# Performance work log

Measured on AMD Instinct MI355X. Metric: run time of the kernel, lower is better.

## Reference

```python
import jax, jax.numpy as jnp
import numpy as np

B, S, D, E, H, TOPK = 4, 2048, 1024, 32, 128, 4

def setup_inputs() -> dict:
    key = jax.random.key(0)
    k1, k2, k3, k4 = jax.random.split(key, 4)
    x = jax.random.normal(k1, (B, S, D), jnp.float32)
    expert_sel = jax.random.normal(k2, (E, D), jnp.float32) * (D ** -0.5)
    keys = jax.random.normal(k3, (E, D, H), jnp.float32) * (D ** -0.5)
    values = jax.random.normal(k4, (E, H, D), jnp.float32) * (H ** -0.5)
    return {"x": x, "expert_sel": expert_sel, "keys": keys, "values": values, "n_heads": TOPK}

def reference(x, expert_sel, keys, values, n_heads):
    # x: [B,S,D]; expert_sel: [E,D]; keys: [E,D,H]; values: [E,H,D]
    Bv, Sv, Dv = x.shape
    Ev = keys.shape[0]
    xf = x.reshape(-1, Dv)                                  # [N,D]
    N = xf.shape[0]
    gate = jax.nn.sigmoid(xf @ expert_sel.T)                # [N,E] sigmoid gating (sigma-MoE)
    vals, idx = jax.lax.top_k(gate, n_heads)                # [N,k] selected experts + gate weights
    # dense per-token-per-expert gate weights; zero for non-selected experts
    g = jnp.zeros((N, Ev), x.dtype).at[jnp.arange(N)[:, None], idx].set(vals)  # [N,E]
    # grouped expert FFN, expressed densely over the (small) expert axis:
    # out = sum_e g[n,e] * relu(x @ keys[e]) @ values[e]
    h = jax.nn.relu(jnp.einsum('nd,edh->enh', xf, keys))    # [E,N,H]
    out = jnp.einsum('enh,ehd->nd', h * g.T[:, :, None], values)  # [N,D]
    return out.reshape(Bv, Sv, Dv)
```

## Files before the change

kernel.cpp:

```cpp
#include <hip/hip_runtime.h>
#include <hip/hip_bf16.h>

#define NTOK 8192
#define DDIM 1024
#define NEXP 32
#define HDIM 128
#define TOPK 4

typedef __attribute__((ext_vector_type(8))) short bf16x8;
typedef __attribute__((ext_vector_type(4))) float f32x4;

typedef unsigned int uint_g __attribute__((address_space(1)));
typedef unsigned int uint_l __attribute__((address_space(3)));

__device__ __forceinline__ void async_cp16(const void* g, void* l) {
    __builtin_amdgcn_global_load_lds((const uint_g*)g, (uint_l*)l, 16, 0, 0);
}

__device__ inline unsigned short f2bf(float f) {
    unsigned int u = __builtin_bit_cast(unsigned int, f);
    unsigned int r = (u + 0x7fffu + ((u >> 16) & 1u)) >> 16;
    return (unsigned short)r;
}
__device__ inline float bf2f(unsigned short s) {
    unsigned int u = ((unsigned int)s) << 16;
    return __builtin_bit_cast(float, u);
}

__global__ __launch_bounds__(256) void prep_weights(
    const float* __restrict__ keys, const float* __restrict__ values,
    unsigned short* __restrict__ Kb, unsigned short* __restrict__ Vb)
{
    int idx = blockIdx.x * 256 + threadIdx.x;
    unsigned short o[8];
    if (idx < NEXP * 128 * 128) {
        int n = idx & 127, k0 = (idx >> 7) & 127, e = idx >> 14;
        const float* s = keys + ((size_t)e * DDIM + k0 * 8) * HDIM + n;
        #pragma unroll
        for (int j = 0; j < 8; ++j) o[j] = f2bf(s[(size_t)j * HDIM]);
        *(uint4*)&Kb[(size_t)idx * 8] = *(uint4*)o;
    } else {
        idx -= NEXP * 128 * 128;
        int n = idx & 1023, k0 = (idx >> 10) & 15, e = idx >> 14;
        const float* s = values + ((size_t)e * HDIM + k0 * 8) * DDIM + n;
        #pragma unroll
        for (int j = 0; j < 8; ++j) o[j] = f2bf(s[(size_t)j * DDIM]);
        *(uint4*)&Vb[(size_t)idx * 8] = *(uint4*)o;
    }
}

__global__ __launch_bounds__(256) void gate_partial(
    const float* __restrict__ x, const float* __restrict__ es,
    float* __restrict__ gpart)
{
    const int n0    = blockIdx.x * 16;
    const int dbase = blockIdx.y * 256;
    const int tid   = threadIdx.x;

    __shared__ float smem[4608];
    float* Xt  = smem;
    float* Est = smem + 64 * 36;

    const int t4  = (tid & 3) * 4;
    const int e4  = ((tid >> 2) & 7) * 4;
    const int rep = tid >> 5;

    const int xr = tid & 15, xc4 = (tid >> 4) * 4;
    const int er = tid & 31, ec8 = (tid >> 5) * 8;

    float acc[4][4] = {};

    for (int dc = dbase; dc < dbase + 256; dc += 64) {
        __syncthreads();
        {
            float4 v = *(const float4*)&x[(size_t)(n0 + xr) * DDIM + dc + xc4];
            Xt[(xc4 + 0) * 36 + xr] = v.x; Xt[(xc4 + 1) * 36 + xr] = v.y;
            Xt[(xc4 + 2) * 36 + xr] = v.z; Xt[(xc4 + 3) * 36 + xr] = v.w;
        }
        #pragma unroll
        for (int i = 0; i < 2; ++i) {
            float4 v = *(const float4*)&es[(size_t)er * DDIM + dc + ec8 + i * 4];
            Est[(ec8 + i * 4 + 0) * 36 + er] = v.x;
            Est[(ec8 + i * 4 + 1) * 36 + er] = v.y;
            Est[(ec8 + i * 4 + 2) * 36 + er] = v.z;
            Est[(ec8 + i * 4 + 3) * 36 + er] = v.w;
        }
        __syncthreads();

        #pragma unroll
        for (int s = 0; s < 8; ++s) {
            int d = s * 8 + rep;
            float4 xv = *(const float4*)&Xt[d * 36 + t4];
            float4 ev = *(const float4*)&Est[d * 36 + e4];
            const float xa[4] = {xv.x, xv.y, xv.z, xv.w};
            const float ea[4] = {ev.x, ev.y, ev.z, ev.w};
            #pragma unroll
            for (int i = 0; i < 4; ++i)
                #pragma unroll
                for (int j = 0; j < 4; ++j)
                    acc[i][j] = fmaf(xa[i], ea[j], acc[i][j]);
        }
    }

    __syncthreads();
    float* Lp = smem;
    #pragma unroll
    for (int i = 0; i < 4; ++i)
        #pragma unroll
        for (int j = 0; j < 4; ++j)
            Lp[(rep * 16 + t4 + i) * 33 + e4 + j] = acc[i][j];
    __syncthreads();

    for (int p = tid; p < 16 * 32; p += 256) {
        int tok = p >> 5, e = p & 31;
        float s = 0.f;
        #pragma unroll
        for (int r = 0; r < 8; ++r) s += Lp[(r * 16 + tok) * 33 + e];
        gpart[((size_t)blockIdx.y * NTOK + n0 + tok) * NEXP + e] = s;
    }
}

__global__ __launch_bounds__(256) void topk_scatter(
    const float* __restrict__ gpart,
    int* __restrict__ cnt, int* __restrict__ tok_list, float* __restrict__ gates)
{
    const int tid = threadIdx.x;
    const int n   = blockIdx.x * 256 + tid;

    __shared__ int hist[NEXP];
    __shared__ int bbase[NEXP];
    if (tid < NEXP) hist[tid] = 0;

    float lg[NEXP];
    #pragma unroll
    for (int i = 0; i < 8; ++i) {
        float4 v = *(const float4*)&gpart[(size_t)n * NEXP + i * 4];
        lg[i*4+0] = v.x; lg[i*4+1] = v.y; lg[i*4+2] = v.z; lg[i*4+3] = v.w;
    }
    #pragma unroll
    for (int j = 1; j < 4; ++j)
        #pragma unroll
        for (int i = 0; i < 8; ++i) {
            float4 v = *(const float4*)&gpart[((size_t)j * NTOK + n) * NEXP + i * 4];
            lg[i*4+0] += v.x; lg[i*4+1] += v.y; lg[i*4+2] += v.z; lg[i*4+3] += v.w;
        }

    int sel[TOPK]; float sv[TOPK];
    #pragma unroll
    for (int j = 0; j < TOPK; ++j) {
        float bv = -3.0e38f; int bi = 0;
        #pragma unroll
        for (int e = 0; e < NEXP; ++e) {
            bool taken = false;
            #pragma unroll
            for (int q = 0; q < j; ++q) taken = taken || (sel[q] == e);
            float v = taken ? -3.0e38f : lg[e];
            if (v > bv) { bv = v; bi = e; }
        }
        sel[j] = bi; sv[j] = bv;
    }

    __syncthreads();
    int lpos[TOPK];
    #pragma unroll
    for (int j = 0; j < TOPK; ++j) {
        gates[n * TOPK + j] = 1.f / (1.f + expf(-sv[j]));
        lpos[j] = atomicAdd(&hist[sel[j]], 1);
    }
    __syncthreads();
    if (tid < NEXP) bbase[tid] = atomicAdd(&cnt[tid], hist[tid]);
    __syncthreads();
    #pragma unroll
    for (int j = 0; j < TOPK; ++j)
        tok_list[(size_t)sel[j] * NTOK + bbase[sel[j]] + lpos[j]] = n * TOPK + j;
}

__global__ __launch_bounds__(256) void ffn_phase1(
    const float* __restrict__ x,
    const unsigned short* __restrict__ Kb,
    const int* __restrict__ cnt, const int* __restrict__ tok_list,
    const float* __restrict__ gates,
    unsigned short* __restrict__ Hb)
{
    const int e = blockIdx.y, tile = blockIdx.x;
    const int c = cnt[e], base = tile * 32;
    if (base >= c) return;
    const int nt   = min(32, c - base);
    const int tid  = threadIdx.x, wave = tid >> 6, lane = tid & 63;
    const int lm   = lane & 15, quad = lane >> 4;
    const int r2   = (wave >> 1) * 16, c2 = (wave & 1) * 64;

    __shared__ __align__(16) unsigned short Xs[32 * 72];
    __shared__ __align__(16) unsigned short Ks[8192];
    __shared__ int slot[32];
    __shared__ int toks[32];
    __shared__ float gs[32];

    if (tid < 32) {
        if (tid < nt) {
            int v = tok_list[(size_t)e * NTOK + base + tid];
            slot[tid] = v; toks[tid] = v >> 2; gs[tid] = gates[v];
        } else { slot[tid] = -1; toks[tid] = -1; gs[tid] = 0.f; }
    }
    __syncthreads();

    const unsigned short* Ke = Kb + (size_t)e * 131072;
    const int xr = tid >> 3, xseg = (tid & 7) * 8;
    const int xtok = toks[xr];
    const float* xrow = x + (size_t)(xtok < 0 ? 0 : xtok) * DDIM;

    f32x4 acc[4];
    #pragma unroll
    for (int j = 0; j < 4; ++j) acc[j] = (f32x4){0.f, 0.f, 0.f, 0.f};

    for (int dc = 0; dc < DDIM; dc += 64) {
        __syncthreads();
        #pragma unroll
        for (int i = 0; i < 4; ++i) {
            int u = wave * 4 + i;
            async_cp16(Ke + (size_t)dc * 128 + u * 512 + lane * 8, Ks + u * 512);
        }
        {
            float4 v0 = make_float4(0.f,0.f,0.f,0.f), v1 = v0;
            if (xtok >= 0) {
                v0 = *(const float4*)&xrow[dc + xseg];
                v1 = *(const float4*)&xrow[dc + xseg + 4];
            }
            unsigned short p[8] = { f2bf(v0.x), f2bf(v0.y), f2bf(v0.z), f2bf(v0.w),
                                    f2bf(v1.x), f2bf(v1.y), f2bf(v1.z), f2bf(v1.w) };
            *(uint4*)&Xs[xr * 72 + xseg] = *(uint4*)p;
        }
        __syncthreads();

        #pragma unroll
        for (int ks = 0; ks < 2; ++ks) {
            bf16x8 a = *(const bf16x8*)&Xs[(r2 + lm) * 72 + ks * 32 + quad * 8];
            #pragma unroll
            for (int tj = 0; tj < 4; ++tj) {
                bf16x8 b = *(const bf16x8*)&Ks[((ks * 4 + quad) * 128 + c2 + tj * 16 + lm) * 8];
                acc[tj] = __builtin_amdgcn_mfma_f32_16x16x32_bf16(a, b, acc[tj], 0, 0, 0);
            }
        }
    }

    #pragma unroll
    for (int reg = 0; reg < 4; ++reg) {
        int m = r2 + quad * 4 + reg;
        int s = slot[m];
        if (s >= 0) {
            float g = gs[m];
            unsigned short* hp = Hb + (size_t)s * HDIM;
            #pragma unroll
            for (int tj = 0; tj < 4; ++tj)
                hp[c2 + tj * 16 + lm] = f2bf(fmaxf(acc[tj][reg], 0.f) * g);
        }
    }
}

__global__ __launch_bounds__(256) void ffn_phase2(
    const unsigned short* __restrict__ Hb,
    const unsigned short* __restrict__ Vb,
    const int* __restrict__ cnt, const int* __restrict__ tok_list,
    unsigned short* __restrict__ Ob)
{
    const int e = blockIdx.z, nc = blockIdx.y, tile = blockIdx.x;
    const int c = cnt[e], base = tile * 64;
    if (base >= c) return;
    const int nt   = min(64, c - base);
    const int tid  = threadIdx.x, wave = tid >> 6, lane = tid & 63;
    const int lm   = lane & 15, quad = lane >> 4;
    const int r2   = (wave >> 1) * 32, c2 = (wave & 1) * 64;

    __shared__ __align__(16) unsigned short Hs[64 * 136];
    __shared__ __align__(16) unsigned short Vs[16384];
    __shared__ int slot[64];

    if (tid < 64) {
        if (tid < nt) slot[tid] = tok_list[(size_t)e * NTOK + base + tid];
        else          slot[tid] = -1;
    }
    __syncthreads();

    const unsigned short* Ve = Vb + (size_t)e * 131072;
    #pragma unroll
    for (int i = 0; i < 8; ++i) {
        int u = wave * 8 + i;
        int k0 = u >> 1, half = u & 1;
        async_cp16(Ve + ((size_t)k0 * 1024 + nc * 128 + half * 64 + lane) * 8,
                   Vs + u * 512);
    }
    {
        const int hr = tid >> 2, part = tid & 3;
        int s = slot[hr];
        uint4 z = {0u, 0u, 0u, 0u};
        uint4 d0 = z, d1 = z, d2 = z, d3 = z;
        if (s >= 0) {
            const uint4* src = (const uint4*)(Hb + (size_t)s * HDIM + part * 32);
            d0 = src[0]; d1 = src[1]; d2 = src[2]; d3 = src[3];
        }
        uint4* dst = (uint4*)&Hs[hr * 136 + part * 32];
        dst[0] = d0; dst[1] = d1; dst[2] = d2; dst[3] = d3;
    }
    __syncthreads();

    f32x4 acc[2][4];
    #pragma unroll
    for (int i = 0; i < 2; ++i)
        #pragma unroll
        for (int j = 0; j < 4; ++j) acc[i][j] = (f32x4){0.f, 0.f, 0.f, 0.f};

    #pragma unroll
    for (int ks = 0; ks < 4; ++ks) {
        bf16x8 a0 = *(const bf16x8*)&Hs[(r2 + lm) * 136 + ks * 32 + quad * 8];
        bf16x8 a1 = *(const bf16x8*)&Hs[(r2 + 16 + lm) * 136 + ks * 32 + quad * 8];
        #pragma unroll
        for (int tj = 0; tj < 4; ++tj) {
            bf16x8 b = *(const bf16x8*)&Vs[((ks * 4 + quad) * 128 + c2 + tj * 16 + lm) * 8];
            acc[0][tj] = __builtin_amdgcn_mfma_f32_16x16x32_bf16(a0, b, acc[0][tj], 0, 0, 0);
            acc[1][tj] = __builtin_amdgcn_mfma_f32_16x16x32_bf16(a1, b, acc[1][tj], 0, 0, 0);
        }
    }

    #pragma unroll
    for (int ti = 0; ti < 2; ++ti)
        #pragma unroll
        for (int reg = 0; reg < 4; ++reg) {
            int m = r2 + ti * 16 + quad * 4 + reg;
            int s = slot[m];
            if (s >= 0) {
                unsigned short* op = Ob + (size_t)s * DDIM + nc * 128 + c2 + lm;
                #pragma unroll
                for (int tj = 0; tj < 4; ++tj)
                    op[tj * 16] = f2bf(acc[ti][tj][reg]);
            }
        }
}

__global__ __launch_bounds__(256) void reduce_out(
    const unsigned short* __restrict__ Ob, float* __restrict__ out)
{
    const int tid = threadIdx.x;
    const int n   = blockIdx.x * 2 + (tid >> 7);
    const int cc  = (tid & 127) * 8;

    float s[8] = {};
    #pragma unroll
    for (int j = 0; j < 4; ++j) {
        uint4 v = *(const uint4*)&Ob[((size_t)n * 4 + j) * DDIM + cc];
        const unsigned int w[4] = {v.x, v.y, v.z, v.w};
        #pragma unroll
        for (int q = 0; q < 4; ++q) {
            s[q * 2 + 0] += bf2f((unsigned short)(w[q] & 0xffff));
            s[q * 2 + 1] += bf2f((unsigned short)(w[q] >> 16));
        }
    }
    float4 o0 = {s[0], s[1], s[2], s[3]};
    float4 o1 = {s[4], s[5], s[6], s[7]};
    *(float4*)&out[(size_t)n * DDIM + cc]     = o0;
    *(float4*)&out[(size_t)n * DDIM + cc + 4] = o1;
}

extern "C" void kernel_launch(void* const* d_in, const int* in_sizes, int n_in,
                              void* d_out, int out_size, void* d_ws, size_t ws_size,
                              hipStream_t stream) {
    const float* x      = (const float*)d_in[0];
    const float* es     = (const float*)d_in[1];
    const float* keys   = (const float*)d_in[2];
    const float* values = (const float*)d_in[3];
    float* out          = (float*)d_out;

    char* w = (char*)d_ws;
    int*   cnt      = (int*)w;               w += 256;
    int*   tok_list = (int*)w;               w += (size_t)NEXP * NTOK * sizeof(int);
    float* gates    = (float*)w;             w += (size_t)NTOK * TOPK * sizeof(float);
    float* gpart    = (float*)w;             w += (size_t)4 * NTOK * NEXP * sizeof(float);
    unsigned short* Kb = (unsigned short*)w; w += (size_t)NEXP * 128 * 128 * 8 * 2;
    unsigned short* Vb = (unsigned short*)w; w += (size_t)NEXP * 16 * 1024 * 8 * 2;
    unsigned short* Hb = (unsigned short*)w; w += (size_t)NTOK * TOPK * HDIM * 2;
    unsigned short* Ob = (unsigned short*)w;

    hipMemsetAsync(cnt, 0, NEXP * sizeof(int), stream);

    prep_weights<<<4096, 256, 0, stream>>>(keys, values, Kb, Vb);
    gate_partial<<<dim3(NTOK / 16, 4), 256, 0, stream>>>(x, es, gpart);
    topk_scatter<<<NTOK / 256, 256, 0, stream>>>(gpart, cnt, tok_list, gates);

    ffn_phase1<<<dim3(64, NEXP), 256, 0, stream>>>(x, Kb, cnt, tok_list, gates, Hb);
    ffn_phase2<<<dim3(32, 8, NEXP), 256, 0, stream>>>(Hb, Vb, cnt, tok_list, Ob);
    reduce_out<<<NTOK / 2, 256, 0, stream>>>(Ob, out);
}
```

Measured before the change: 221.1 us.

## Pre-convert x to bf16 and double-buffer async loads in both FFN phases

x is converted to bf16 once in the prep kernel, into a buffer that aliases Ob, so phase 1 gathers token rows with async global-to-LDS copies instead of converting per tile. Phase 1 now uses 64-token tiles with double-buffered K and X stages. Phase 2 drops the separate column-block grid dimension: each block keeps its H tile in LDS and loops over all 1024 output columns with a double-buffered V stream. The goal is to overlap loads with MFMA work and avoid re-reading H across column blocks, at the cost of fewer, longer blocks and some added LDS use.

New measurement: 251.8 us. 13.9% more time.

```diff
diff --git a/kernel.cpp b/kernel.cpp
--- a/kernel.cpp
+++ b/kernel.cpp
@@ -28,8 +28,10 @@
 }
 
 __global__ __launch_bounds__(256) void prep_weights(
+    const float* __restrict__ x,
     const float* __restrict__ keys, const float* __restrict__ values,
-    unsigned short* __restrict__ Kb, unsigned short* __restrict__ Vb)
+    unsigned short* __restrict__ Kb, unsigned short* __restrict__ Vb,
+    unsigned short* __restrict__ Xb)
 {
     int idx = blockIdx.x * 256 + threadIdx.x;
     unsigned short o[8];
@@ -39,13 +41,19 @@
         #pragma unroll
         for (int j = 0; j < 8; ++j) o[j] = f2bf(s[(size_t)j * HDIM]);
         *(uint4*)&Kb[(size_t)idx * 8] = *(uint4*)o;
-    } else {
+    } else if (idx < 2 * NEXP * 128 * 128) {
         idx -= NEXP * 128 * 128;
         int n = idx & 1023, k0 = (idx >> 10) & 15, e = idx >> 14;
         const float* s = values + ((size_t)e * HDIM + k0 * 8) * DDIM + n;
         #pragma unroll
         for (int j = 0; j < 8; ++j) o[j] = f2bf(s[(size_t)j * DDIM]);
         *(uint4*)&Vb[(size_t)idx * 8] = *(uint4*)o;
+    } else {
+        idx -= 2 * NEXP * 128 * 128;
+        const float* s = x + (size_t)idx * 8;
+        #pragma unroll
+        for (int j = 0; j < 8; ++j) o[j] = f2bf(s[j]);
+        *(uint4*)&Xb[(size_t)idx * 8] = *(uint4*)o;
     }
 }
 
@@ -176,94 +184,13 @@
 }
 
 __global__ __launch_bounds__(256) void ffn_phase1(
-    const float* __restrict__ x,
+    const unsigned short* __restrict__ Xb,
     const unsigned short* __restrict__ Kb,
     const int* __restrict__ cnt, const int* __restrict__ tok_list,
     const float* __restrict__ gates,
     unsigned short* __restrict__ Hb)
 {
     const int e = blockIdx.y, tile = blockIdx.x;
-    const int c = cnt[e], base = tile * 32;
-    if (base >= c) return;
-    const int nt   = min(32, c - base);
-    const int tid  = threadIdx.x, wave = tid >> 6, lane = tid & 63;
-    const int lm   = lane & 15, quad = lane >> 4;
-    const int r2   = (wave >> 1) * 16, c2 = (wave & 1) * 64;
-
-    __shared__ __align__(16) unsigned short Xs[32 * 72];
-    __shared__ __align__(16) unsigned short Ks[8192];
-    __shared__ int slot[32];
-    __shared__ int toks[32];
-    __shared__ float gs[32];
-
-    if (tid < 32) {
-        if (tid < nt) {
-            int v = tok_list[(size_t)e * NTOK + base + tid];
-            slot[tid] = v; toks[tid] = v >> 2; gs[tid] = gates[v];
-        } else { slot[tid] = -1; toks[tid] = -1; gs[tid] = 0.f; }
-    }
-    __syncthreads();
-
-    const unsigned short* Ke = Kb + (size_t)e * 131072;
-    const int xr = tid >> 3, xseg = (tid & 7) * 8;
-    const int xtok = toks[xr];
-    const float* xrow = x + (size_t)(xtok < 0 ? 0 : xtok) * DDIM;
-
-    f32x4 acc[4];
-    #pragma unroll
-    for (int j = 0; j < 4; ++j) acc[j] = (f32x4){0.f, 0.f, 0.f, 0.f};
-
-    for (int dc = 0; dc < DDIM; dc += 64) {
-        __syncthreads();
-        #pragma unroll
-        for (int i = 0; i < 4; ++i) {
-            int u = wave * 4 + i;
-            async_cp16(Ke + (size_t)dc * 128 + u * 512 + lane * 8, Ks + u * 512);
-        }
-        {
-            float4 v0 = make_float4(0.f,0.f,0.f,0.f), v1 = v0;
-            if (xtok >= 0) {
-                v0 = *(const float4*)&xrow[dc + xseg];
-                v1 = *(const float4*)&xrow[dc + xseg + 4];
-            }
-            unsigned short p[8] = { f2bf(v0.x), f2bf(v0.y), f2bf(v0.z), f2bf(v0.w),
-                                    f2bf(v1.x), f2bf(v1.y), f2bf(v1.z), f2bf(v1.w) };
-            *(uint4*)&Xs[xr * 72 + xseg] = *(uint4*)p;
-        }
-        __syncthreads();
-
-        #pragma unroll
-        for (int ks = 0; ks < 2; ++ks) {
-            bf16x8 a = *(const bf16x8*)&Xs[(r2 + lm) * 72 + ks * 32 + quad * 8];
-            #pragma unroll
-            for (int tj = 0; tj < 4; ++tj) {
-                bf16x8 b = *(const bf16x8*)&Ks[((ks * 4 + quad) * 128 + c2 + tj * 16 + lm) * 8];
-                acc[tj] = __builtin_amdgcn_mfma_f32_16x16x32_bf16(a, b, acc[tj], 0, 0, 0);
-            }
-        }
-    }
-
-    #pragma unroll
-    for (int reg = 0; reg < 4; ++reg) {
-        int m = r2 + quad * 4 + reg;
-        int s = slot[m];
-        if (s >= 0) {
-            float g = gs[m];
-            unsigned short* hp = Hb + (size_t)s * HDIM;
-            #pragma unroll
-            for (int tj = 0; tj < 4; ++tj)
-                hp[c2 + tj * 16 + lm] = f2bf(fmaxf(acc[tj][reg], 0.f) * g);
-        }
-    }
-}
-
-__global__ __launch_bounds__(256) void ffn_phase2(
-    const unsigned short* __restrict__ Hb,
-    const unsigned short* __restrict__ Vb,
-    const int* __restrict__ cnt, const int* __restrict__ tok_list,
-    unsigned short* __restrict__ Ob)
-{
-    const int e = blockIdx.z, nc = blockIdx.y, tile = blockIdx.x;
     const int c = cnt[e], base = tile * 64;
     if (base >= c) return;
     const int nt   = min(64, c - base);
@@ -271,37 +198,20 @@
     const int lm   = lane & 15, quad = lane >> 4;
     const int r2   = (wave >> 1) * 32, c2 = (wave & 1) * 64;
 
-    __shared__ __align__(16) unsigned short Hs[64 * 136];
-    __shared__ __align__(16) unsigned short Vs[16384];
-    __shared__ int slot[64];
+    __shared__ __align__(16) unsigned short Ks[2][8192];
+    __shared__ __align__(16) unsigned short Xs[2][4096];
+    __shared__ int slot[64]; __shared__ int gtok[64]; __shared__ float gs[64];
 
     if (tid < 64) {
-        if (tid < nt) slot[tid] = tok_list[(size_t)e * NTOK + base + tid];
-        else          slot[tid] = -1;
-    }
-    __syncthreads();
-
-    const unsigned short* Ve = Vb + (size_t)e * 131072;
-    #pragma unroll
-    for (int i = 0; i < 8; ++i) {
-        int u = wave * 8 + i;
-        int k0 = u >> 1, half = u & 1;
-        async_cp16(Ve + ((size_t)k0 * 1024 + nc * 128 + half * 64 + lane) * 8,
-                   Vs + u * 512);
-    }
-    {
-        const int hr = tid >> 2, part = tid & 3;
-        int s = slot[hr];
-        uint4 z = {0u, 0u, 0u, 0u};
-        uint4 d0 = z, d1 = z, d2 = z, d3 = z;
-        if (s >= 0) {
-            const uint4* src = (const uint4*)(Hb + (size_t)s * HDIM + part * 32);
-            d0 = src[0]; d1 = src[1]; d2 = src[2]; d3 = src[3];
-        }
-        uint4* dst = (uint4*)&Hs[hr * 136 + part * 32];
-        dst[0] = d0; dst[1] = d1; dst[2] = d2; dst[3] = d3;
-    }
-    __syncthreads();
+        if (tid < nt) {
+            int v = tok_list[(size_t)e * NTOK + base + tid];
+            slot[tid] = v; gtok[tid] = v >> 2; gs[tid] = gates[v];
+        } else { slot[tid] = -1; gtok[tid] = 0; gs[tid] = 0.f; }
+    }
+    __syncthreads();
+
+    const unsigned short* Ke   = Kb + (size_t)e * 131072;
+    const unsigned short* xrow = Xb + (size_t)gtok[lane] * DDIM;
 
     f32x4 acc[2][4];
     #pragma unroll
@@ -309,16 +219,40 @@
         #pragma unroll
         for (int j = 0; j < 4; ++j) acc[i][j] = (f32x4){0.f, 0.f, 0.f, 0.f};
 
-    #pragma unroll
-    for (int ks = 0; ks < 4; ++ks) {
-        bf16x8 a0 = *(const bf16x8*)&Hs[(r2 + lm) * 136 + ks * 32 + quad * 8];
-        bf16x8 a1 = *(const bf16x8*)&Hs[(r2 + 16 + lm) * 136 + ks * 32 + quad * 8];
-        #pragma unroll
-        for (int tj = 0; tj < 4; ++tj) {
-            bf16x8 b = *(const bf16x8*)&Vs[((ks * 4 + quad) * 128 + c2 + tj * 16 + lm) * 8];
-            acc[0][tj] = __builtin_amdgcn_mfma_f32_16x16x32_bf16(a0, b, acc[0][tj], 0, 0, 0);
-            acc[1][tj] = __builtin_amdgcn_mfma_f32_16x16x32_bf16(a1, b, acc[1][tj], 0, 0, 0);
-        }
+    auto stage = [&](int t, int b) {
+        int dc = t * 64;
+        #pragma unroll
+        for (int i = 0; i < 4; ++i) {
+            int p = wave * 4 + i;
+            async_cp16(Ke + ((size_t)(dc / 8 + (p >> 1)) * 128 + (p & 1) * 64 + lane) * 8,
+                       &Ks[b][p * 512]);
+        }
+        #pragma unroll
+        for (int i = 0; i < 2; ++i) {
+            int k0 = wave * 2 + i;
+            async_cp16(xrow + dc + k0 * 8, &Xs[b][k0 * 512]);
+        }
+    };
+
+    stage(0, 0);
+    __syncthreads();
+
+    for (int t = 0; t < 16; ++t) {
+        int b = t & 1;
+        if (t < 15) stage(t + 1, b ^ 1);
+        #pragma unroll
+        for (int ks = 0; ks < 2; ++ks) {
+            int k0 = ks * 4 + quad;
+            bf16x8 a0 = *(const bf16x8*)&Xs[b][(k0 * 64 + r2 + lm) * 8];
+            bf16x8 a1 = *(const bf16x8*)&Xs[b][(k0 * 64 + r2 + 16 + lm) * 8];
+            #pragma unroll
+            for (int tj = 0; tj < 4; ++tj) {
+                bf16x8 bb = *(const bf16x8*)&Ks[b][(k0 * 128 + c2 + tj * 16 + lm) * 8];
+                acc[0][tj] = __builtin_amdgcn_mfma_f32_16x16x32_bf16(a0, bb, acc[0][tj], 0, 0, 0);
+                acc[1][tj] = __builtin_amdgcn_mfma_f32_16x16x32_bf16(a1, bb, acc[1][tj], 0, 0, 0);
+            }
+        }
+        __syncthreads();
     }
 
     #pragma unroll
@@ -328,12 +262,95 @@
             int m = r2 + ti * 16 + quad * 4 + reg;
             int s = slot[m];
             if (s >= 0) {
-                unsigned short* op = Ob + (size_t)s * DDIM + nc * 128 + c2 + lm;
+                float g = gs[m];
+                unsigned short* hp = Hb + (size_t)s * HDIM;
                 #pragma unroll
                 for (int tj = 0; tj < 4; ++tj)
-                    op[tj * 16] = f2bf(acc[ti][tj][reg]);
+                    hp[c2 + tj * 16 + lm] = f2bf(fmaxf(acc[ti][tj][reg], 0.f) * g);
             }
         }
+}
+
+__global__ __launch_bounds__(256) void ffn_phase2(
+    const unsigned short* __restrict__ Hb,
+    const unsigned short* __restrict__ Vb,
+    const int* __restrict__ cnt, const int* __restrict__ tok_list,
+    unsigned short* __restrict__ Ob)
+{
+    const int e = blockIdx.y, tile = blockIdx.x;
+    const int c = cnt[e], base = tile * 64;
+    if (base >= c) return;
+    const int nt   = min(64, c - base);
+    const int tid  = threadIdx.x, wave = tid >> 6, lane = tid & 63;
+    const int lm   = lane & 15, quad = lane >> 4;
+    const int r2   = (wave >> 1) * 32, cw = (wave & 1) * 32;
+
+    __shared__ __align__(16) unsigned short Hs[8192];
+    __shared__ __align__(16) unsigned short Vs[2][8192];
+    __shared__ int slot[64]; __shared__ int gslot[64];
+
+    if (tid < 64) {
+        int v = (tid < nt) ? tok_list[(size_t)e * NTOK + base + tid] : -1;
+        slot[tid] = v; gslot[tid] = v < 0 ? 0 : v;
+    }
+    __syncthreads();
+
+    const unsigned short* Ve   = Vb + (size_t)e * 131072;
+    const unsigned short* hrow = Hb + (size_t)gslot[lane] * HDIM;
+
+    auto stageV = [&](int cc, int b) {
+        #pragma unroll
+        for (int i = 0; i < 4; ++i) {
+            int k0 = wave * 4 + i;
+            async_cp16(Ve + ((size_t)k0 * 1024 + cc * 64 + lane) * 8, &Vs[b][k0 * 512]);
+        }
+    };
+
+    #pragma unroll
+    for (int i = 0; i < 4; ++i) {
+        int k0 = wave * 4 + i;
+        async_cp16(hrow + k0 * 8, &Hs[k0 * 512]);
+    }
+    stageV(0, 0);
+    __syncthreads();
+
+    for (int cc = 0; cc < 16; ++cc) {
+        int b = cc & 1;
+        if (cc < 15) stageV(cc + 1, b ^ 1);
+
+        f32x4 acc[2][2];
+        #pragma unroll
+        for (int i = 0; i < 2; ++i)
+            #pragma unroll
+            for (int j = 0; j < 2; ++j) acc[i][j] = (f32x4){0.f, 0.f, 0.f, 0.f};
+
+        #pragma unroll
+        for (int ks = 0; ks < 4; ++ks) {
+            int k0 = ks * 4 + quad;
+            bf16x8 a0 = *(const bf16x8*)&Hs[(k0 * 64 + r2 + lm) * 8];
+            bf16x8 a1 = *(const bf16x8*)&Hs[(k0 * 64 + r2 + 16 + lm) * 8];
+            #pragma unroll
+            for (int tj = 0; tj < 2; ++tj) {
+                bf16x8 bb = *(const bf16x8*)&Vs[b][(k0 * 64 + cw + tj * 16 + lm) * 8];
+                acc[0][tj] = __builtin_amdgcn_mfma_f32_16x16x32_bf16(a0, bb, acc[0][tj], 0, 0, 0);
+                acc[1][tj] = __builtin_amdgcn_mfma_f32_16x16x32_bf16(a1, bb, acc[1][tj], 0, 0, 0);
+            }
+        }
+
+        #pragma unroll
+        for (int ti = 0; ti < 2; ++ti)
+            #pragma unroll
+            for (int reg = 0; reg < 4; ++reg) {
+                int m = r2 + ti * 16 + quad * 4 + reg;
+                int s = slot[m];
+                if (s >= 0) {
+                    unsigned short* op = Ob + (size_t)s * DDIM + cc * 64 + cw + lm;
+                    op[0]  = f2bf(acc[ti][0][reg]);
+                    op[16] = f2bf(acc[ti][1][reg]);
+                }
+            }
+        __syncthreads();
+    }
 }
 
 __global__ __launch_bounds__(256) void reduce_out(
@@ -378,14 +395,15 @@
     unsigned short* Vb = (unsigned short*)w; w += (size_t)NEXP * 16 * 1024 * 8 * 2;
     unsigned short* Hb = (unsigned short*)w; w += (size_t)NTOK * TOPK * HDIM * 2;
     unsigned short* Ob = (unsigned short*)w;
+    unsigned short* Xb = Ob;
 
     hipMemsetAsync(cnt, 0, NEXP * sizeof(int), stream);
 
-    prep_weights<<<4096, 256, 0, stream>>>(keys, values, Kb, Vb);
+    prep_weights<<<8192, 256, 0, stream>>>(x, keys, values, Kb, Vb, Xb);
     gate_partial<<<dim3(NTOK / 16, 4), 256, 0, stream>>>(x, es, gpart);
     topk_scatter<<<NTOK / 256, 256, 0, stream>>>(gpart, cnt, tok_list, gates);
 
-    ffn_phase1<<<dim3(64, NEXP), 256, 0, stream>>>(x, Kb, cnt, tok_list, gates, Hb);
-    ffn_phase2<<<dim3(32, 8, NEXP), 256, 0, stream>>>(Hb, Vb, cnt, tok_list, Ob);
+    ffn_phase1<<<dim3(64, NEXP), 256, 0, stream>>>(Xb, Kb, cnt, tok_list, gates, Hb);
+    ffn_phase2<<<dim3(64, NEXP), 256, 0, stream>>>(Hb, Vb, cnt, tok_list, Ob);
     reduce_out<<<NTOK / 2, 256, 0, stream>>>(Ob, out);
 }
```
